# Performance work log

Measured on AMD Instinct MI355X. Metric: run time of the kernel, lower is better.

The kernel has to match this reference:

```python
import jax, jax.numpy as jnp
import numpy as np

B, L, NIN, NHID, NLAYERS = 16, 2048, 1024, 1024, 2


def _gru_step_zero_h(x, W_ih, b_ih, W_hh, b_hh):
    """torch GRU cell with h_prev = 0 (faithful to the module's bug where
    hidden is never updated and starts at zeros).
    r = sigmoid(W_ir x + b_ir + b_hr)
    z = sigmoid(W_iz x + b_iz + b_hz)
    n = tanh(W_in x + b_in + r * b_hn)   # W_hn @ 0 == 0
    h = (1 - z) * n                       # + z * 0
    W_hh is unused because h_prev == 0 (kept as an arg for parity).
    """
    del W_hh
    g = jnp.einsum('blf,hf->blh', x, W_ih) + b_ih  # (B, L, 3H)
    H = b_ih.shape[0] // 3
    gi_r, gi_z, gi_n = g[..., :H], g[..., H:2 * H], g[..., 2 * H:]
    bh_r, bh_z, bh_n = b_hh[:H], b_hh[H:2 * H], b_hh[2 * H:]
    r = jax.nn.sigmoid(gi_r + bh_r)
    z = jax.nn.sigmoid(gi_z + bh_z)
    n = jnp.tanh(gi_n + r * bh_n)
    return (1.0 - z) * n


def setup_inputs() -> dict:
    key = jax.random.key(0)
    ks = jax.random.split(key, 12)
    s_in = 1.0 / np.sqrt(NIN)
    s_h = 1.0 / np.sqrt(NHID)
    inp = {
        'inputs': jax.random.normal(ks[0], (B, L, NIN), dtype=jnp.float32),
        'inputs_mask': jax.random.randint(ks[1], (B, L), 0, 2, dtype=jnp.int32),
        # layer 0 (input size NIN)
        'W_ih0': jax.random.uniform(ks[2], (3 * NHID, NIN), jnp.float32, -s_in, s_in),
        'W_hh0': jax.random.uniform(ks[3], (3 * NHID, NHID), jnp.float32, -s_h, s_h),
        'b_ih0': jax.random.uniform(ks[4], (3 * NHID,), jnp.float32, -s_h, s_h),
        'b_hh0': jax.random.uniform(ks[5], (3 * NHID,), jnp.float32, -s_h, s_h),
        # layer 1 (input size NHID)
        'W_ih1': jax.random.uniform(ks[6], (3 * NHID, NHID), jnp.float32, -s_h, s_h),
        'W_hh1': jax.random.uniform(ks[7], (3 * NHID, NHID), jnp.float32, -s_h, s_h),
        'b_ih1': jax.random.uniform(ks[8], (3 * NHID,), jnp.float32, -s_h, s_h),
        'b_hh1': jax.random.uniform(ks[9], (3 * NHID,), jnp.float32, -s_h, s_h),
    }
    return inp


def reference(inputs, inputs_mask, W_ih0, W_hh0, b_ih0, b_hh0,
              W_ih1, W_hh1, b_ih1, b_hh1):
    # hidden is never updated in the original step(), so every timestep runs
    # the 2-layer GRU one step from zero hidden -> fully parallel over time.
    h1 = _gru_step_zero_h(inputs, W_ih0, b_ih0, W_hh0, b_hh0)   # (B, L, H)
    h2 = _gru_step_zero_h(h1, W_ih1, b_ih1, W_hh1, b_hh1)       # (B, L, H)
    mask = inputs_mask.astype(h2.dtype)[..., None]               # (B, L, 1)
    # output_p * mask + hidden[0] * (1 - mask), with hidden[0] == 0
    out = h2 * mask
    # original returns (steps, b_s, nhid)
    return jnp.transpose(out, (1, 0, 2))
```

## Files before the change

kernel.cpp:

```cpp
#include <hip/hip_runtime.h>
#include <hip/hip_bf16.h>
#include <cstdint>
#include <cstddef>

#define BB 16
#define LL 2048
#define MM (BB * LL)
#define KK 1024
#define HH 1024

typedef __attribute__((ext_vector_type(8))) short bf16x8;
typedef __attribute__((ext_vector_type(4))) float f32x4;

__device__ __forceinline__ unsigned short f2bf(float f) {
    unsigned u = __builtin_bit_cast(unsigned, f);
    u += 0x7fffu + ((u >> 16) & 1u);
    return (unsigned short)(u >> 16);
}

__global__ void cvt_f32_to_bf16(const float* __restrict__ in,
                                unsigned short* __restrict__ out, int n8) {
    int i = blockIdx.x * blockDim.x + threadIdx.x;
    if (i >= n8) return;
    const float4* p = reinterpret_cast<const float4*>(in) + (size_t)i * 2;
    float4 v0 = p[0];
    float4 v1 = p[1];
    union { unsigned short us[8]; uint4 v; } o;
    o.us[0] = f2bf(v0.x); o.us[1] = f2bf(v0.y);
    o.us[2] = f2bf(v0.z); o.us[3] = f2bf(v0.w);
    o.us[4] = f2bf(v1.x); o.us[5] = f2bf(v1.y);
    o.us[6] = f2bf(v1.z); o.us[7] = f2bf(v1.w);
    reinterpret_cast<uint4*>(out)[i] = o.v;
}

__global__ __launch_bounds__(1024) void scan_mask(const int* __restrict__ mask,
                                                  int* __restrict__ rows,
                                                  int* __restrict__ Na) {
    __shared__ int psum[1024];
    const int t = threadIdx.x;
    const int base = t * 32;
    int m[32];
    int cnt = 0;
#pragma unroll
    for (int i = 0; i < 32; ++i) { m[i] = mask[base + i]; cnt += (m[i] != 0); }
    psum[t] = cnt;
    __syncthreads();
    for (int off = 1; off < 1024; off <<= 1) {
        int v = (t >= off) ? psum[t - off] : 0;
        __syncthreads();
        psum[t] += v;
        __syncthreads();
    }
    int offset = psum[t] - cnt;
#pragma unroll
    for (int i = 0; i < 32; ++i) {
        if (m[i]) rows[offset++] = base + i;
    }
    if (t == 1023) *Na = psum[1023];
}

__global__ __launch_bounds__(256) void gather_cvt(const float* __restrict__ x,
                                                  const int* __restrict__ rows,
                                                  const int* __restrict__ Na,
                                                  unsigned short* __restrict__ xbf) {
    const int j = blockIdx.x;
    if (j >= *Na) return;
    const int r = rows[j];
    const float4 v = reinterpret_cast<const float4*>(x + (size_t)r * KK)[threadIdx.x];
    ushort4 o;
    o.x = f2bf(v.x); o.y = f2bf(v.y); o.z = f2bf(v.z); o.w = f2bf(v.w);
    reinterpret_cast<ushort4*>(xbf + (size_t)j * KK)[threadIdx.x] = o;
}

__global__ __launch_bounds__(256) void zero_masked(const int* __restrict__ mask,
                                                   float* __restrict__ out) {
    const int m = blockIdx.x;
    if (mask[m] != 0) return;
    const int bb = m >> 11;
    const int ll = m & 2047;
    float4 z = {0.f, 0.f, 0.f, 0.f};
    reinterpret_cast<float4*>(out + ((size_t)ll * BB + bb) * HH)[threadIdx.x] = z;
}

__device__ __forceinline__ void gload16(const unsigned short* g, unsigned short* l) {
    __builtin_amdgcn_global_load_lds(
        (const __attribute__((address_space(1))) unsigned int*)g,
        (__attribute__((address_space(3))) unsigned int*)l,
        16, 0, 0);
}

#define WAITVM0 asm volatile("s_waitcnt vmcnt(0)" ::: "memory")
#define SB      __builtin_amdgcn_sched_barrier(0)
#define BAR     __builtin_amdgcn_s_barrier()

template <int MODE>
__global__ __launch_bounds__(256, 2) void gru_layer(
    const unsigned short* __restrict__ A,
    const unsigned short* __restrict__ W,
    const float* __restrict__ b_ih,
    const float* __restrict__ b_hh,
    const int* __restrict__ rows,
    const int* __restrict__ Na_p,
    unsigned short* __restrict__ out_bf,
    float* __restrict__ out_f) {
    __shared__ unsigned short lds[2][10240];

    const int Na = *Na_p;
    const int m0 = blockIdx.x * 128;
    if (m0 >= Na) return;
    const int n0 = blockIdx.y * 64;

    const int tid  = threadIdx.x;
    const int lane = tid & 63;
    const int wid  = tid >> 6;
    const int wr   = wid >> 1;
    const int wc   = wid & 1;

    const int trow = tid >> 2;
    const int tcol = ((tid & 3) ^ (trow & 3)) * 8;
    int r0 = m0 + trow;        if (r0 >= Na) r0 = Na - 1;
    int r1 = m0 + 64 + trow;   if (r1 >= Na) r1 = Na - 1;
    const unsigned short* a0 = A + (size_t)r0 * KK + tcol;
    const unsigned short* a1 = A + (size_t)r1 * KK + tcol;
    const unsigned short* b0 = W + (size_t)(0 * HH + n0 + trow) * KK + tcol;
    const unsigned short* b1 = W + (size_t)(1 * HH + n0 + trow) * KK + tcol;
    const unsigned short* b2 = W + (size_t)(2 * HH + n0 + trow) * KK + tcol;

#define STAGE(kt, c) do {                                        \
        const int _o = (kt) * 32;                                \
        unsigned short* _L = &lds[(c)][wid * 512];               \
        gload16(a0 + _o, _L + 0 * 2048);                         \
        gload16(a1 + _o, _L + 1 * 2048);                         \
        gload16(b0 + _o, _L + 2 * 2048);                         \
        gload16(b1 + _o, _L + 3 * 2048);                         \
        gload16(b2 + _o, _L + 4 * 2048);                         \
    } while (0)

    const int l15 = lane & 15;
    const int akp = (((lane >> 4) ^ (lane & 3)) & 3) << 3;
    int aoff[4], boff[2];
#pragma unroll
    for (int mf = 0; mf < 4; ++mf)
        aoff[mf] = (wr * 64 + mf * 16 + l15) * 32 + akp;
#pragma unroll
    for (int nf = 0; nf < 2; ++nf)
        boff[nf] = 4096 + (wc * 32 + nf * 16 + l15) * 32 + akp;

    f32x4 accr[4][2] = {};
    f32x4 accz[4][2] = {};
    f32x4 accn[4][2] = {};

#define COMPUTE(Lp) do {                                                          \
        bf16x8 af[4];                                                             \
        _Pragma("unroll") for (int mf = 0; mf < 4; ++mf)                          \
            af[mf] = *reinterpret_cast<const bf16x8*>(&(Lp)[aoff[mf]]);           \
        _Pragma("unroll") for (int nf = 0; nf < 2; ++nf) {                        \
            bf16x8 br  = *reinterpret_cast<const bf16x8*>(&(Lp)[boff[nf]]);       \
            bf16x8 bz  = *reinterpret_cast<const bf16x8*>(&(Lp)[boff[nf] + 2048]);\
            bf16x8 bnn = *reinterpret_cast<const bf16x8*>(&(Lp)[boff[nf] + 4096]);\
            __builtin_amdgcn_s_setprio(1);                                        \
            _Pragma("unroll") for (int mf = 0; mf < 4; ++mf) {                    \
                accr[mf][nf] = __builtin_amdgcn_mfma_f32_16x16x32_bf16(           \
                    af[mf], br,  accr[mf][nf], 0, 0, 0);                          \
                accz[mf][nf] = __builtin_amdgcn_mfma_f32_16x16x32_bf16(           \
                    af[mf], bz,  accz[mf][nf], 0, 0, 0);                          \
                accn[mf][nf] = __builtin_amdgcn_mfma_f32_16x16x32_bf16(           \
                    af[mf], bnn, accn[mf][nf], 0, 0, 0);                          \
            }                                                                     \
            __builtin_amdgcn_s_setprio(0);                                        \
        }                                                                         \
    } while (0)

    STAGE(0, 0);
    WAITVM0; BAR; SB;

    int cur = 0;
#pragma unroll 1
    for (int kt = 0; kt < 31; ++kt) {
        STAGE(kt + 1, cur ^ 1);
        const unsigned short* L = &lds[cur][0];
        COMPUTE(L);
        WAITVM0; BAR; SB;
        cur ^= 1;
    }
    {
        const unsigned short* L = &lds[cur][0];
        COMPUTE(L);
    }

#pragma unroll
    for (int nf = 0; nf < 2; ++nf) {
        const int col = n0 + wc * 32 + nf * 16 + l15;
        const float br_b = b_ih[col] + b_hh[col];
        const float bz_b = b_ih[HH + col] + b_hh[HH + col];
        const float bn_i = b_ih[2 * HH + col];
        const float bn_h = b_hh[2 * HH + col];
#pragma unroll
        for (int mf = 0; mf < 4; ++mf) {
#pragma unroll
            for (int j = 0; j < 4; ++j) {
                const int row = m0 + wr * 64 + mf * 16 + (lane >> 4) * 4 + j;
                if (row >= Na) continue;
                const float r = 1.f / (1.f + __expf(-(accr[mf][nf][j] + br_b)));
                const float z = 1.f / (1.f + __expf(-(accz[mf][nf][j] + bz_b)));
                const float n = tanhf(accn[mf][nf][j] + bn_i + r * bn_h);
                const float h = (1.f - z) * n;
                if (MODE == 0) {
                    out_bf[(size_t)row * HH + col] = f2bf(h);
                } else {
                    const int orig = rows[row];
                    const int bb = orig >> 11;
                    const int ll = orig & 2047;
                    out_f[((size_t)ll * BB + bb) * HH + col] = h;
                }
            }
        }
    }
#undef STAGE
#undef COMPUTE
}

extern "C" void kernel_launch(void* const* d_in, const int* in_sizes, int n_in,
                              void* d_out, int out_size, void* d_ws, size_t ws_size,
                              hipStream_t stream) {
    const float* x   = (const float*)d_in[0];
    const int*   msk = (const int*)d_in[1];
    const float* W0  = (const float*)d_in[2];
    const float* bi0 = (const float*)d_in[4];
    const float* bh0 = (const float*)d_in[5];
    const float* W1  = (const float*)d_in[6];
    const float* bi1 = (const float*)d_in[8];
    const float* bh1 = (const float*)d_in[9];
    float* out = (float*)d_out;

    char* ws = (char*)d_ws;
    unsigned short* xbf  = (unsigned short*)ws;
    unsigned short* h1bf = (unsigned short*)(ws + 67108864);
    unsigned short* w0bf = (unsigned short*)(ws + 134217728);
    unsigned short* w1bf = (unsigned short*)(ws + 140509184);
    int* rows = (int*)(ws + 146800640);
    int* Na   = (int*)(ws + 146931712);

    scan_mask<<<1, 1024, 0, stream>>>(msk, rows, Na);

    cvt_f32_to_bf16<<<1536, 256, 0, stream>>>(W0, w0bf, 3 * HH * KK / 8);
    cvt_f32_to_bf16<<<1536, 256, 0, stream>>>(W1, w1bf, 3 * HH * KK / 8);

    zero_masked<<<MM, 256, 0, stream>>>(msk, out);
    gather_cvt<<<MM, 256, 0, stream>>>(x, rows, Na, xbf);

    dim3 grid(MM / 128, HH / 64);
    gru_layer<0><<<grid, 256, 0, stream>>>(xbf, w0bf, bi0, bh0, rows, Na, h1bf, nullptr);
    gru_layer<1><<<grid, 256, 0, stream>>>(h1bf, w1bf, bi1, bh1, rows, Na, nullptr, out);
}
```

Baseline: 350.3 us.

## Triple-buffer LDS pipeline with partial vmcnt waits and revised swizzle

Replaces the double-buffered global-to-LDS pipeline with a three-stage ring buffer that prefetches two tiles ahead. It waits only on the oldest outstanding loads through partial vmcnt counts, so memory latency can overlap with more than one compute step. It also changes the XOR swizzle of the K-chunk to use row bits shifted by one, aiming to reduce LDS bank conflicts. The extra LDS (60KB per block) may reduce occupancy below the two blocks per CU targeted by the launch bounds, and the loop adds a second barrier per iteration.

```diff
diff --git a/kernel.cpp b/kernel.cpp
--- a/kernel.cpp
+++ b/kernel.cpp
@@ -89,9 +89,12 @@
         16, 0, 0);
 }
 
-#define WAITVM0 asm volatile("s_waitcnt vmcnt(0)" ::: "memory")
-#define SB      __builtin_amdgcn_sched_barrier(0)
-#define BAR     __builtin_amdgcn_s_barrier()
+#define WAITVM10 asm volatile("s_waitcnt vmcnt(10)" ::: "memory")
+#define WAITVM5  asm volatile("s_waitcnt vmcnt(5)" ::: "memory")
+#define WAITVM0  asm volatile("s_waitcnt vmcnt(0)" ::: "memory")
+#define WAITLG0  asm volatile("s_waitcnt lgkmcnt(0)" ::: "memory")
+#define SB       __builtin_amdgcn_sched_barrier(0)
+#define BAR      __builtin_amdgcn_s_barrier()
 
 template <int MODE>
 __global__ __launch_bounds__(256, 2) void gru_layer(
@@ -103,7 +106,7 @@
     const int* __restrict__ Na_p,
     unsigned short* __restrict__ out_bf,
     float* __restrict__ out_f) {
-    __shared__ unsigned short lds[2][10240];
+    __shared__ unsigned short lds[3 * 10240];
 
     const int Na = *Na_p;
     const int m0 = blockIdx.x * 128;
@@ -117,7 +120,7 @@
     const int wc   = wid & 1;
 
     const int trow = tid >> 2;
-    const int tcol = ((tid & 3) ^ (trow & 3)) * 8;
+    const int tcol = ((tid & 3) ^ ((trow >> 1) & 3)) * 8;
     int r0 = m0 + trow;        if (r0 >= Na) r0 = Na - 1;
     int r1 = m0 + 64 + trow;   if (r1 >= Na) r1 = Na - 1;
     const unsigned short* a0 = A + (size_t)r0 * KK + tcol;
@@ -126,9 +129,9 @@
     const unsigned short* b1 = W + (size_t)(1 * HH + n0 + trow) * KK + tcol;
     const unsigned short* b2 = W + (size_t)(2 * HH + n0 + trow) * KK + tcol;
 
-#define STAGE(kt, c) do {                                        \
+#define STAGE(kt, Lbase) do {                                    \
         const int _o = (kt) * 32;                                \
-        unsigned short* _L = &lds[(c)][wid * 512];               \
+        unsigned short* _L = (Lbase) + wid * 512;                \
         gload16(a0 + _o, _L + 0 * 2048);                         \
         gload16(a1 + _o, _L + 1 * 2048);                         \
         gload16(b0 + _o, _L + 2 * 2048);                         \
@@ -137,7 +140,7 @@
     } while (0)
 
     const int l15 = lane & 15;
-    const int akp = (((lane >> 4) ^ (lane & 3)) & 3) << 3;
+    const int akp = (((lane >> 4) ^ (lane >> 1)) & 3) << 3;
     int aoff[4], boff[2];
 #pragma unroll
     for (int mf = 0; mf < 4; ++mf)
@@ -171,22 +174,29 @@
         }                                                                         \
     } while (0)
 
-    STAGE(0, 0);
+    STAGE(0, &lds[0]);
+    STAGE(1, &lds[10240]);
+    STAGE(2, &lds[20480]);
+
+    int cur = 0;
+    unsigned short* Lc = &lds[0];
+#pragma unroll 1
+    for (int kt = 0; kt < 29; ++kt) {
+        WAITVM10; BAR; SB;
+        COMPUTE(Lc);
+        WAITLG0; BAR; SB;
+        STAGE(kt + 3, Lc);
+        cur = (cur == 2) ? 0 : cur + 1;
+        Lc = &lds[cur * 10240];
+    }
+    WAITVM10; BAR; SB;
+    COMPUTE(Lc);
+    cur = (cur == 2) ? 0 : cur + 1; Lc = &lds[cur * 10240];
+    WAITVM5; BAR; SB;
+    COMPUTE(Lc);
+    cur = (cur == 2) ? 0 : cur + 1; Lc = &lds[cur * 10240];
     WAITVM0; BAR; SB;
-
-    int cur = 0;
-#pragma unroll 1
-    for (int kt = 0; kt < 31; ++kt) {
-        STAGE(kt + 1, cur ^ 1);
-        const unsigned short* L = &lds[cur][0];
-        COMPUTE(L);
-        WAITVM0; BAR; SB;
-        cur ^= 1;
-    }
-    {
-        const unsigned short* L = &lds[cur][0];
-        COMPUTE(L);
-    }
+    COMPUTE(Lc);
 
 #pragma unroll
     for (int nf = 0; nf < 2; ++nf) {
```

Result: slower. 372.3 us (+6.3%).
